# Performance work log

Measured on AMD Instinct MI355X. Metric: run time of the kernel, lower is better.

Reference implementation:

```python
import jax, jax.numpy as jnp
import numpy as np
import math

D = 128    # d_model
H = 8      # n_heads
NK = 16    # n_know
BS = 4
S = 256
DK = D // H
NEG = -1e32
LN_EPS = 1e-5


def _linear(x, W, b):
    return x @ W.T + b


def _layernorm(x, g, b):
    m = x.mean(-1, keepdims=True)
    v = ((x - m) ** 2).mean(-1, keepdims=True)
    return (x - m) / jnp.sqrt(v + LN_EPS) * g + b


def _attention(q, k, v, mask, gamma, maxout):
    # q,k,v: (B, H, S, DK); mask: (1,1,S,S) bool; gamma: (H,1,1)
    d_k = q.shape[-1]
    scores = jnp.einsum('bhid,bhjd->bhij', q, k) / math.sqrt(d_k)
    seqlen = scores.shape[-1]
    x = jnp.arange(seqlen, dtype=jnp.float32)
    pos = jnp.abs(x[None, :] - x[:, None])  # |j - i|, (S, S)
    # --- time-decay block (computed under no_grad in torch) ---
    s_ = jax.nn.softmax(jnp.where(mask, scores, NEG), axis=-1)
    distcum = jnp.cumsum(s_, axis=-1)
    disttotal = jnp.sum(s_, axis=-1, keepdims=True)
    dist = jnp.sqrt(jnp.clip((disttotal - distcum) * pos[None, None], 0.0, None))
    dist = jax.lax.stop_gradient(dist)
    effect = jnp.clip(jnp.exp(dist * (-jnp.abs(gamma)[None])), 1e-5, 1e5)
    scores = scores * effect
    scores = jax.nn.softmax(jnp.where(mask, scores, NEG), axis=-1)
    scores = jnp.where(mask, scores, 0.0)
    if maxout:
        scale = jnp.minimum(1.0 / scores.max(axis=-1, keepdims=True), 5.0)
        scores = scores * scale
    out = jnp.einsum('bhij,bhjd->bhid', scores, v)
    return out, scores


def _mha(q, k, v, mask, Wq, bq, Wk, bk, Wv, bv, Wo, bo, gamma, maxout):
    bs, seqlen, d = q.shape
    split = lambda x: x.reshape(bs, seqlen, H, DK).transpose(0, 2, 1, 3)
    qh = split(_linear(q, Wq, bq))
    kh = split(_linear(k, Wk, bk))
    vh = split(_linear(v, Wv, bv))
    out, scores = _attention(qh, kh, vh, mask, gamma, maxout)
    concat = out.transpose(0, 2, 1, 3).reshape(bs, seqlen, d)
    return _linear(concat, Wo, bo), scores


def _layer(query, key, values, peek_cur, Wq, bq, Wk, bk, Wv, bv, Wo, bo, gamma, lng, lnb):
    seqlen = query.shape[1]
    mask = jnp.tril(jnp.ones((seqlen, seqlen), bool), 0 if peek_cur else -1)[None, None]
    out, scores = _mha(query, key, values, mask, Wq, bq, Wk, bk, Wv, bv, Wo, bo, gamma,
                       maxout=not peek_cur)
    return _layernorm(query + out, lng, lnb), scores


def setup_inputs() -> dict:
    key = jax.random.key(0)
    ks = jax.random.split(key, 24)
    rn = lambda k, shape: (jax.random.normal(k, shape, jnp.float32) / math.sqrt(D))
    inp = {
        'q_emb': jax.random.normal(ks[0], (BS, S, D), jnp.float32),
        's_emb': jax.random.normal(ks[1], (BS, S, D), jnp.float32),
        'lens': jax.random.randint(ks[2], (BS,), 5, S),
        # block1 (kq_same=True -> shares Wq for K)
        'b1_Wq': rn(ks[3], (D, D)), 'b1_bq': jnp.zeros((D,), jnp.float32),
        'b1_Wv': rn(ks[4], (D, D)), 'b1_bv': jnp.zeros((D,), jnp.float32),
        'b1_Wo': rn(ks[5], (D, D)), 'b1_bo': jnp.zeros((D,), jnp.float32),
        'b1_gamma': jax.random.uniform(ks[6], (H, 1, 1), jnp.float32, -1.0, 1.0),
        'b1_lng': jnp.ones((D,), jnp.float32), 'b1_lnb': jnp.zeros((D,), jnp.float32),
        # block4 (kq_same=False)
        'b4_Wq': rn(ks[7], (D, D)), 'b4_bq': jnp.zeros((D,), jnp.float32),
        'b4_Wk': rn(ks[8], (D, D)), 'b4_bk': jnp.zeros((D,), jnp.float32),
        'b4_Wv': rn(ks[9], (D, D)), 'b4_bv': jnp.zeros((D,), jnp.float32),
        'b4_Wo': rn(ks[10], (D, D)), 'b4_bo': jnp.zeros((D,), jnp.float32),
        'b4_gamma': jax.random.uniform(ks[11], (H, 1, 1), jnp.float32, -1.0, 1.0),
        'b4_lng': jnp.ones((D,), jnp.float32), 'b4_lnb': jnp.zeros((D,), jnp.float32),
        'know_params': jax.random.uniform(ks[12], (NK, D), jnp.float32, -1.0, 1.0),
    }
    return inp


def reference(q_emb, s_emb, lens,
              b1_Wq, b1_bq, b1_Wv, b1_bv, b1_Wo, b1_bo, b1_gamma, b1_lng, b1_lnb,
              b4_Wq, b4_bq, b4_Wk, b4_bk, b4_Wv, b4_bv, b4_Wo, b4_bo, b4_gamma, b4_lng, b4_lnb,
              know_params):
    # n_layers == 1 path, eval mode (no mask dropout); lens unused in eval math.
    hq = q_emb
    p, q_scores = _layer(q_emb, q_emb, s_emb, True,
                         b1_Wq, b1_bq, b1_Wq, b1_bq, b1_Wv, b1_bv, b1_Wo, b1_bo,
                         b1_gamma, b1_lng, b1_lnb)
    bs, seqlen, d = p.shape
    query = jnp.broadcast_to(know_params[None, :, None, :], (bs, NK, seqlen, d)).reshape(bs * NK, seqlen, d)
    hq_r = jnp.broadcast_to(hq[:, None], (bs, NK, seqlen, d)).reshape(bs * NK, seqlen, d)
    p_r = jnp.broadcast_to(p[:, None], (bs, NK, seqlen, d)).reshape(bs * NK, seqlen, d)
    z, k_scores = _layer(query, hq_r, p_r, False,
                         b4_Wq, b4_bq, b4_Wk, b4_bk, b4_Wv, b4_bv, b4_Wo, b4_bo,
                         b4_gamma, b4_lng, b4_lnb)
    z = z.reshape(bs, NK, seqlen, d).transpose(0, 2, 1, 3).reshape(bs, seqlen, NK * d)
    k_scores = k_scores.reshape(bs, NK, H, seqlen, seqlen).transpose(0, 2, 3, 1, 4)
    return z, q_scores, k_scores
```

## Files before the change

### kernel.cpp

```cpp
#include <hip/hip_runtime.h>

#define DEV __device__ __forceinline__

DEV float4 f4fma(float4 a, float s, float4 w){
  a.x = fmaf(s, w.x, a.x); a.y = fmaf(s, w.y, a.y);
  a.z = fmaf(s, w.z, a.z); a.w = fmaf(s, w.w, a.w);
  return a;
}
DEV float4 f4add(float4 a, float4 b){
  a.x+=b.x; a.y+=b.y; a.z+=b.z; a.w+=b.w; return a;
}

DEV float waveAllMax(float x){
  #pragma unroll
  for(int o=1;o<64;o<<=1) x = fmaxf(x, __shfl_xor(x,o,64));
  return x;
}
DEV float waveAllSum(float x){
  #pragma unroll
  for(int o=1;o<64;o<<=1) x += __shfl_xor(x,o,64);
  return x;
}
DEV float waveReduceMax(float x){
  #pragma unroll
  for(int o=32;o>0;o>>=1) x = fmaxf(x, __shfl_down(x,o,64));
  return x;
}
DEV float blockMax256(float x, float* sc){
  int lane = threadIdx.x & 63, wid = threadIdx.x >> 6;
  x = waveReduceMax(x);
  __syncthreads();
  if(lane==0) sc[wid] = x;
  __syncthreads();
  return fmaxf(fmaxf(sc[0],sc[1]), fmaxf(sc[2],sc[3]));
}
DEV float blockScan256(float x, float* sc, float& total){
  int lane = threadIdx.x & 63, wid = threadIdx.x >> 6;
  float v = x;
  #pragma unroll
  for(int o=1;o<64;o<<=1){ float t = __shfl_up(v,o,64); if(lane>=o) v += t; }
  __syncthreads();
  if(lane==63) sc[wid] = v;
  __syncthreads();
  float pre=0.f, tot=0.f;
  #pragma unroll
  for(int ww=0;ww<4;ww++){ float s = sc[ww]; tot += s; if(ww<wid) pre += s; }
  total = tot;
  return v + pre;
}

template<int EPI>
DEV void gemm16_body(const float* __restrict__ in, const float* __restrict__ W,
                     const float* __restrict__ bias, const float* __restrict__ aux,
                     const float* __restrict__ lng, const float* __restrict__ lnb,
                     float* __restrict__ out, int r0, int nrows,
                     float* sWT, float (*sIn)[128])
{
  const int t = threadIdx.x;
  for(int idx=t; idx<2048; idx+=256){
    int r = idx>>7, c = idx&127;
    int row = r0+r;
    sIn[r][c] = (row<nrows) ? in[(size_t)row*128+c] : 0.f;
  }
  const int og = t & 31, rg = t >> 5;
  const int o0 = og*4;
  const float* s0p = sIn[rg*2];
  const float* s1p = sIn[rg*2+1];
  float4 a0 = make_float4(0,0,0,0), a1 = make_float4(0,0,0,0);

  #pragma unroll
  for(int half=0; half<2; half++){
    int c0 = half*64;
    __syncthreads();
    for(int idx=t; idx<8192; idx+=256){
      int o = idx>>6, cc = idx&63;
      sWT[cc*132 + o] = W[o*128 + c0 + cc];
    }
    __syncthreads();
    #pragma unroll 4
    for(int c=0;c<64;c+=4){
      float4 sA = *(const float4*)(s0p + c0 + c);
      float4 sB = *(const float4*)(s1p + c0 + c);
      const float* wp = sWT + c*132 + o0;
      float4 w0 = *(const float4*)(wp);
      float4 w1 = *(const float4*)(wp + 132);
      float4 w2 = *(const float4*)(wp + 264);
      float4 w3 = *(const float4*)(wp + 396);
      a0 = f4fma(a0, sA.x, w0); a0 = f4fma(a0, sA.y, w1);
      a0 = f4fma(a0, sA.z, w2); a0 = f4fma(a0, sA.w, w3);
      a1 = f4fma(a1, sB.x, w0); a1 = f4fma(a1, sB.y, w1);
      a1 = f4fma(a1, sB.z, w2); a1 = f4fma(a1, sB.w, w3);
    }
  }
  float4 bv = *(const float4*)(bias + o0);
  a0 = f4add(a0, bv); a1 = f4add(a1, bv);
  int row0 = r0 + rg*2, row1 = row0 + 1;

  if(EPI == 0){
    if(row0 < nrows) *(float4*)(out + (size_t)row0*128 + o0) = a0;
    if(row1 < nrows) *(float4*)(out + (size_t)row1*128 + o0) = a1;
  } else {
    const float* x0 = aux + ((row0>>8)&15)*128;
    const float* x1 = aux + ((row1>>8)&15)*128;
    a0 = f4add(a0, *(const float4*)(x0 + o0));
    a1 = f4add(a1, *(const float4*)(x1 + o0));
    float s0 = a0.x+a0.y+a0.z+a0.w, s1 = a1.x+a1.y+a1.z+a1.w;
    float q0 = a0.x*a0.x+a0.y*a0.y+a0.z*a0.z+a0.w*a0.w;
    float q1 = a1.x*a1.x+a1.y*a1.y+a1.z*a1.z+a1.w*a1.w;
    #pragma unroll
    for(int o=1;o<32;o<<=1){
      s0 += __shfl_xor(s0,o,64); q0 += __shfl_xor(q0,o,64);
      s1 += __shfl_xor(s1,o,64); q1 += __shfl_xor(q1,o,64);
    }
    float m0 = s0*0.0078125f, v0 = q0*0.0078125f - m0*m0;
    float m1 = s1*0.0078125f, v1 = q1*0.0078125f - m1*m1;
    float i0 = rsqrtf(v0+1e-5f), i1 = rsqrtf(v1+1e-5f);
    float4 g  = *(const float4*)(lng + o0);
    float4 b2 = *(const float4*)(lnb + o0);
    float4 y0, y1;
    y0.x=(a0.x-m0)*i0*g.x+b2.x; y0.y=(a0.y-m0)*i0*g.y+b2.y;
    y0.z=(a0.z-m0)*i0*g.z+b2.z; y0.w=(a0.w-m0)*i0*g.w+b2.w;
    y1.x=(a1.x-m1)*i1*g.x+b2.x; y1.y=(a1.y-m1)*i1*g.y+b2.y;
    y1.z=(a1.z-m1)*i1*g.z+b2.z; y1.w=(a1.w-m1)*i1*g.w+b2.w;
    int n0=(row0>>8)&15, b0=row0>>12, i0i=row0&255;
    int n1=(row1>>8)&15, b1=row1>>12, i1i=row1&255;
    float* p0 = out + ((((size_t)b0*256+i0i)*16+n0)<<7);
    float* p1 = out + ((((size_t)b1*256+i1i)*16+n1)<<7);
    *(float4*)(p0 + o0) = y0;
    *(float4*)(p1 + o0) = y1;
  }
}

template<int EPI>
__global__ __launch_bounds__(256) void gemm16_kernel(
  const float* __restrict__ in, const float* __restrict__ W,
  const float* __restrict__ bias, const float* __restrict__ aux,
  const float* __restrict__ lng, const float* __restrict__ lnb,
  float* __restrict__ out, int nrows)
{
  __shared__ float sWT[64*132];
  __shared__ float sIn[16][128];
  gemm16_body<EPI>(in, W, bias, aux, lng, lnb, out, blockIdx.x*16, nrows, sWT, sIn);
}

__global__ __launch_bounds__(256) void proj4_kernel(
  const float* __restrict__ in0, const float* __restrict__ W0, const float* __restrict__ b0, float* __restrict__ o0,
  const float* __restrict__ in1, const float* __restrict__ W1, const float* __restrict__ b1, float* __restrict__ o1,
  const float* __restrict__ in2, const float* __restrict__ W2, const float* __restrict__ b2, float* __restrict__ o2,
  const float* __restrict__ in3, const float* __restrict__ W3, const float* __restrict__ b3, float* __restrict__ o3)
{
  __shared__ float sWT[64*132];
  __shared__ float sIn[16][128];
  int bb = blockIdx.x;
  if(bb < 64)       gemm16_body<0>(in0,W0,b0,nullptr,nullptr,nullptr,o0, bb*16,      1024, sWT,sIn);
  else if(bb < 128) gemm16_body<0>(in1,W1,b1,nullptr,nullptr,nullptr,o1,(bb-64)*16,  1024, sWT,sIn);
  else if(bb < 192) gemm16_body<0>(in2,W2,b2,nullptr,nullptr,nullptr,o2,(bb-128)*16, 1024, sWT,sIn);
  else              gemm16_body<0>(in3,W3,b3,nullptr,nullptr,nullptr,o3, 0,          16,   sWT,sIn);
}

__global__ __launch_bounds__(256) void gemm_p_v4(
  const float* __restrict__ in, const float* __restrict__ Wo, const float* __restrict__ bo,
  const float* __restrict__ resid, const float* __restrict__ lng, const float* __restrict__ lnb,
  float* __restrict__ pout,
  const float* __restrict__ Wv, const float* __restrict__ bvv, float* __restrict__ v4out)
{
  __shared__ float sWT[64*132];
  __shared__ float sIn[16][128];
  const int t = threadIdx.x;
  const int r0 = blockIdx.x*16;
  for(int idx=t; idx<2048; idx+=256){
    int r = idx>>7, c = idx&127;
    sIn[r][c] = in[(size_t)(r0+r)*128+c];
  }
  const int og = t & 31, rg = t >> 5;
  const int o0 = og*4;
  const float* s0p = sIn[rg*2];
  const float* s1p = sIn[rg*2+1];
  float4 a0 = make_float4(0,0,0,0), a1 = make_float4(0,0,0,0);

  #pragma unroll
  for(int half=0; half<2; half++){
    int c0 = half*64;
    __syncthreads();
    for(int idx=t; idx<8192; idx+=256){
      int o = idx>>6, cc = idx&63;
      sWT[cc*132 + o] = Wo[o*128 + c0 + cc];
    }
    __syncthreads();
    #pragma unroll 4
    for(int c=0;c<64;c+=4){
      float4 sA = *(const float4*)(s0p + c0 + c);
      float4 sB = *(const float4*)(s1p + c0 + c);
      const float* wp = sWT + c*132 + o0;
      float4 w0 = *(const float4*)(wp);
      float4 w1 = *(const float4*)(wp + 132);
      float4 w2 = *(const float4*)(wp + 264);
      float4 w3 = *(const float4*)(wp + 396);
      a0 = f4fma(a0, sA.x, w0); a0 = f4fma(a0, sA.y, w1);
      a0 = f4fma(a0, sA.z, w2); a0 = f4fma(a0, sA.w, w3);
      a1 = f4fma(a1, sB.x, w0); a1 = f4fma(a1, sB.y, w1);
      a1 = f4fma(a1, sB.z, w2); a1 = f4fma(a1, sB.w, w3);
    }
  }
  int row0 = r0 + rg*2, row1 = row0 + 1;
  {
    float4 bv = *(const float4*)(bo + o0);
    a0 = f4add(a0, bv); a1 = f4add(a1, bv);
    a0 = f4add(a0, *(const float4*)(resid + (size_t)row0*128 + o0));
    a1 = f4add(a1, *(const float4*)(resid + (size_t)row1*128 + o0));
    float s0 = a0.x+a0.y+a0.z+a0.w, s1 = a1.x+a1.y+a1.z+a1.w;
    float q0 = a0.x*a0.x+a0.y*a0.y+a0.z*a0.z+a0.w*a0.w;
    float q1 = a1.x*a1.x+a1.y*a1.y+a1.z*a1.z+a1.w*a1.w;
    #pragma unroll
    for(int o=1;o<32;o<<=1){
      s0 += __shfl_xor(s0,o,64); q0 += __shfl_xor(q0,o,64);
      s1 += __shfl_xor(s1,o,64); q1 += __shfl_xor(q1,o,64);
    }
    float m0 = s0*0.0078125f, v0 = q0*0.0078125f - m0*m0;
    float m1 = s1*0.0078125f, v1 = q1*0.0078125f - m1*m1;
    float i0 = rsqrtf(v0+1e-5f), i1 = rsqrtf(v1+1e-5f);
    float4 g  = *(const float4*)(lng + o0);
    float4 b2 = *(const float4*)(lnb + o0);
    float4 y0, y1;
    y0.x=(a0.x-m0)*i0*g.x+b2.x; y0.y=(a0.y-m0)*i0*g.y+b2.y;
    y0.z=(a0.z-m0)*i0*g.z+b2.z; y0.w=(a0.w-m0)*i0*g.w+b2.w;
    y1.x=(a1.x-m1)*i1*g.x+b2.x; y1.y=(a1.y-m1)*i1*g.y+b2.y;
    y1.z=(a1.z-m1)*i1*g.z+b2.z; y1.w=(a1.w-m1)*i1*g.w+b2.w;
    *(float4*)(pout + (size_t)row0*128 + o0) = y0;
    *(float4*)(pout + (size_t)row1*128 + o0) = y1;
    __syncthreads();
    *(float4*)&sIn[rg*2  ][o0] = y0;
    *(float4*)&sIn[rg*2+1][o0] = y1;
  }

  a0 = make_float4(0,0,0,0); a1 = make_float4(0,0,0,0);
  #pragma unroll
  for(int half=0; half<2; half++){
    int c0 = half*64;
    __syncthreads();
    for(int idx=t; idx<8192; idx+=256){
      int o = idx>>6, cc = idx&63;
      sWT[cc*132 + o] = Wv[o*128 + c0 + cc];
    }
    __syncthreads();
    #pragma unroll 4
    for(int c=0;c<64;c+=4){
      float4 sA = *(const float4*)(s0p + c0 + c);
      float4 sB = *(const float4*)(s1p + c0 + c);
      const float* wp = sWT + c*132 + o0;
      float4 w0 = *(const float4*)(wp);
      float4 w1 = *(const float4*)(wp + 132);
      float4 w2 = *(const float4*)(wp + 264);
      float4 w3 = *(const float4*)(wp + 396);
      a0 = f4fma(a0, sA.x, w0); a0 = f4fma(a0, sA.y, w1);
      a0 = f4fma(a0, sA.z, w2); a0 = f4fma(a0, sA.w, w3);
      a1 = f4fma(a1, sB.x, w0); a1 = f4fma(a1, sB.y, w1);
      a1 = f4fma(a1, sB.z, w2); a1 = f4fma(a1, sB.w, w3);
    }
  }
  float4 bv2 = *(const float4*)(bvv + o0);
  a0 = f4add(a0, bv2); a1 = f4add(a1, bv2);
  *(float4*)(v4out + (size_t)row0*128 + o0) = a0;
  *(float4*)(v4out + (size_t)row1*128 + o0) = a1;
}

__global__ __launch_bounds__(256) void attn1_kernel(
  const float* __restrict__ qk, const float* __restrict__ v1,
  const float* __restrict__ gamma, float* __restrict__ qs, float* __restrict__ aout)
{
  __shared__ float psW[4][256];
  int tile = blockIdx.x & 15;
  int bh   = blockIdx.x >> 4;
  int b = bh >> 3, h = bh & 7;
  int t = threadIdx.x, lane = t & 63, w = t >> 6;
  int d = lane & 15, jg = lane >> 4;
  int j0 = 4*lane;

  float4 kreg[4][4];
  #pragma unroll
  for(int u=0;u<4;u++){
    const float4* kr = (const float4*)(qk + (b*256 + j0 + u)*128 + h*16);
    kreg[u][0]=kr[0]; kreg[u][1]=kr[1]; kreg[u][2]=kr[2]; kreg[u][3]=kr[3];
  }
  float vreg[64];
  const float* vbase = v1 + (b*256 + jg*64)*128 + h*16 + d;
  #pragma unroll
  for(int k=0;k<64;k++) vreg[k] = vbase[k*128];

  float ga = fabsf(gamma[h]);

  for(int r=0;r<4;r++){
    int i = tile*16 + w*4 + r;
    const float4* qr = (const float4*)(qk + (b*256 + i)*128 + h*16);
    float4 q0=qr[0], q1=qr[1], q2=qr[2], q3=qr[3];

    float raw[4]; float mloc = -3e38f;
    #pragma unroll
    for(int u=0;u<4;u++){
      const float4* kk = kreg[u];
      float s = q0.x*kk[0].x + q0.y*kk[0].y + q0.z*kk[0].z + q0.w*kk[0].w
              + q1.x*kk[1].x + q1.y*kk[1].y + q1.z*kk[1].z + q1.w*kk[1].w
              + q2.x*kk[2].x + q2.y*kk[2].y + q2.z*kk[2].z + q2.w*kk[2].w
              + q3.x*kk[3].x + q3.y*kk[3].y + q3.z*kk[3].z + q3.w*kk[3].w;
      raw[u] = s * 0.25f;
      if(j0+u <= i) mloc = fmaxf(mloc, raw[u]);
    }
    float m1 = waveAllMax(mloc);
    float e[4], c[4]; float lsum = 0.f;
    #pragma unroll
    for(int u=0;u<4;u++){
      e[u] = (j0+u <= i) ? __expf(raw[u]-m1) : 0.f;
      lsum += e[u]; c[u] = lsum;
    }
    float s = lsum;
    #pragma unroll
    for(int o=1;o<64;o<<=1){ float tv = __shfl_up(s,o,64); if(lane>=o) s += tv; }
    float pre = s - lsum;
    float tot = __shfl(s, 63, 64);
    float invtot = 1.f/tot;

    float s2v[4]; float m2loc = -3e38f;
    #pragma unroll
    for(int u=0;u<4;u++){
      int j = j0+u;
      float cum  = (pre + c[u]) * invtot;
      float remn = fmaxf(1.f - cum, 0.f);
      float dist = sqrtf(remn * fabsf((float)(j - i)));
      float eff  = fminf(fmaxf(__expf(-ga*dist), 1e-5f), 1e5f);
      s2v[u] = raw[u]*eff;
      if(j <= i) m2loc = fmaxf(m2loc, s2v[u]);
    }
    float m2 = waveAllMax(m2loc);
    float e2[4]; float zloc = 0.f;
    #pragma unroll
    for(int u=0;u<4;u++){
      e2[u] = (j0+u <= i) ? __expf(s2v[u]-m2) : 0.f;
      zloc += e2[u];
    }
    float Z = waveAllSum(zloc);
    float invZ = 1.f/Z;
    float p0=e2[0]*invZ, p1=e2[1]*invZ, p2=e2[2]*invZ, p3=e2[3]*invZ;

    *(float4*)(qs + ((size_t)(bh*256 + i))*256 + j0) = make_float4(p0,p1,p2,p3);

    *(float4*)&psW[w][j0] = make_float4(p0,p1,p2,p3);
    float acc = 0.f;
    const float4* pw = (const float4*)&psW[w][jg*64];
    #pragma unroll
    for(int k=0;k<16;k++){
      float4 pk = pw[k];
      acc += pk.x*vreg[4*k] + pk.y*vreg[4*k+1] + pk.z*vreg[4*k+2] + pk.w*vreg[4*k+3];
    }
    acc += __shfl_xor(acc,16,64);
    acc += __shfl_xor(acc,32,64);
    if(lane < 16)
      aout[(b*256 + i)*128 + h*16 + d] = acc;
  }
}

DEV float dot16(const float* a, const float* b){
  float s = 0.f;
  #pragma unroll
  for(int k=0;k<16;k++) s += a[k]*b[k];
  return s;
}

__global__ __launch_bounds__(256) void attn4_main(
  const float* __restrict__ q4, const float* __restrict__ k4,
  const float* __restrict__ v4, const float* __restrict__ gamma,
  float* __restrict__ ks, float* __restrict__ aout)
{
  __shared__ float sc4[4];
  __shared__ float rawL[256];
  __shared__ float PL[256];
  __shared__ float psW[4][256];
  int half = blockIdx.x & 1;
  int bnh  = blockIdx.x >> 1;
  int b = bnh >> 7, n = (bnh >> 3) & 15, h = bnh & 7;
  int t = threadIdx.x, lane = t & 63, w = t >> 6;
  int d = lane & 15, jg = lane >> 4;
  int j0 = 4*lane;

  {
    const float* qrow = q4 + n*128 + h*16;
    const float* krow = k4 + (b*256 + t)*128 + h*16;
    float raw = dot16(qrow, krow) * 0.25f;
    float M = blockMax256(raw, sc4);
    float E = __expf(raw - M);
    float tot;
    float P = blockScan256(E, sc4, tot);
    rawL[t] = raw;
    PL[t]   = P;
  }
  float vreg[64];
  const float* vbase = v4 + (b*256 + jg*64)*128 + h*16 + d;
  #pragma unroll
  for(int k=0;k<64;k++) vreg[k] = vbase[k*128];
  __syncthreads();

  float4 rw = *(const float4*)(rawL + j0);
  float4 Pv = *(const float4*)(PL + j0);
  float P_[4] = {Pv.x, Pv.y, Pv.z, Pv.w};
  float R_[4] = {rw.x, rw.y, rw.z, rw.w};

  float g4a = fabsf(gamma[h]);
  size_t ksrowbase = ((size_t)(b*8 + h)*256)*4096 + (size_t)n*256 + j0;

  for(int r=0;r<32;r++){
    int i = half*128 + w*32 + r;
    float p0=0.f,p1=0.f,p2=0.f,p3=0.f;
    if(i > 0){
      float invPm1 = 1.f / PL[i-1];
      float s2v[4]; float mloc = -3e38f;
      #pragma unroll
      for(int u=0;u<4;u++){
        int j = j0+u;
        float cum  = P_[u]*invPm1;
        float remn = fmaxf(1.f - cum, 0.f);
        float dist = sqrtf(remn * fabsf((float)(j - i)));
        float eff  = fminf(fmaxf(__expf(-g4a*dist), 1e-5f), 1e5f);
        float s2   = R_[u]*eff;
        s2v[u] = s2;
        if(j < i) mloc = fmaxf(mloc, s2);
      }
      float m2 = waveAllMax(mloc);
      float e_[4]; float zloc = 0.f;
      #pragma unroll
      for(int u=0;u<4;u++){
        float e = (j0+u < i) ? __expf(s2v[u]-m2) : 0.f;
        e_[u] = e; zloc += e;
      }
      float Z = waveAllSum(zloc);
      float sc = fminf(5.f/Z, 1.f);
      p0=e_[0]*sc; p1=e_[1]*sc; p2=e_[2]*sc; p3=e_[3]*sc;
    }
    *(float4*)(ks + ksrowbase + (size_t)i*4096) = make_float4(p0,p1,p2,p3);

    *(float4*)&psW[w][j0] = make_float4(p0,p1,p2,p3);
    float acc = 0.f;
    const float4* pw = (const float4*)&psW[w][jg*64];
    #pragma unroll
    for(int k=0;k<16;k++){
      float4 pk = pw[k];
      acc += pk.x*vreg[4*k] + pk.y*vreg[4*k+1] + pk.z*vreg[4*k+2] + pk.w*vreg[4*k+3];
    }
    acc += __shfl_xor(acc,16,64);
    acc += __shfl_xor(acc,32,64);
    if(lane < 16)
      aout[((b*16+n)*256 + i)*128 + h*16 + d] = acc;
  }
}

extern "C" void kernel_launch(void* const* d_in, const int* in_sizes, int n_in,
                              void* d_out, int out_size, void* d_ws, size_t ws_size,
                              hipStream_t stream)
{
  (void)in_sizes; (void)n_in; (void)out_size; (void)ws_size;
  const float* q_emb   = (const float*)d_in[0];
  const float* s_emb   = (const float*)d_in[1];
  const float* b1_Wq   = (const float*)d_in[3];
  const float* b1_bq   = (const float*)d_in[4];
  const float* b1_Wv   = (const float*)d_in[5];
  const float* b1_bv   = (const float*)d_in[6];
  const float* b1_Wo   = (const float*)d_in[7];
  const float* b1_bo   = (const float*)d_in[8];
  const float* b1_gamma= (const float*)d_in[9];
  const float* b1_lng  = (const float*)d_in[10];
  const float* b1_lnb  = (const float*)d_in[11];
  const float* b4_Wq   = (const float*)d_in[12];
  const float* b4_bq   = (const float*)d_in[13];
  const float* b4_Wk   = (const float*)d_in[14];
  const float* b4_bk   = (const float*)d_in[15];
  const float* b4_Wv   = (const float*)d_in[16];
  const float* b4_bv   = (const float*)d_in[17];
  const float* b4_Wo   = (const float*)d_in[18];
  const float* b4_bo   = (const float*)d_in[19];
  const float* b4_gamma= (const float*)d_in[20];
  const float* b4_lng  = (const float*)d_in[21];
  const float* b4_lnb  = (const float*)d_in[22];
  const float* know    = (const float*)d_in[23];

  float* w    = (float*)d_ws;
  float* qk1  = w;
  float* v1   = w + 131072;
  float* a1o  = w + 262144;
  float* p    = w + 393216;
  float* q4   = w + 524288;
  float* k4   = w + 526336;
  float* v4   = w + 657408;
  float* a4o  = w + 788480;

  float* z_out  = (float*)d_out;
  float* qs_out = z_out + 2097152;
  float* ks_out = z_out + 4194304;

  proj4_kernel<<<193,256,0,stream>>>(
      q_emb, b1_Wq, b1_bq, qk1,
      s_emb, b1_Wv, b1_bv, v1,
      q_emb, b4_Wk, b4_bk, k4,
      know,  b4_Wq, b4_bq, q4);

  attn1_kernel<<<512,256,0,stream>>>(qk1, v1, b1_gamma, qs_out, a1o);

  gemm_p_v4<<<64,256,0,stream>>>(a1o, b1_Wo, b1_bo, q_emb, b1_lng, b1_lnb, p,
                                 b4_Wv, b4_bv, v4);

  attn4_main<<<1024,256,0,stream>>>(q4, k4, v4, b4_gamma, ks_out, a4o);

  gemm16_kernel<2><<<1024,256,0,stream>>>(a4o, b4_Wo, b4_bo, know, b4_lng, b4_lnb, z_out, 16384);
}
```

Measured before the change: 305.0 us.

## Vectorize P·V with float4 V registers and split attn4 rows into quarters

In both attention kernels the P·V product now has each lane hold 16 consecutive key rows times 4 head dims as float4, instead of 64 strided scalars. Probabilities go to padded shared memory (stride 20) to avoid bank conflicts, and a float4 shuffle reduction across 16 lane groups produces the output, written as one float4. This replaces 64 strided scalar loads with 16 vector loads. attn4 also splits each (b,n,h) across 4 blocks instead of 2, doubling the grid to 2048. That adds parallelism but repeats the per-block prefix scan and V load more often, and the reduction needs more shuffles.

```diff
diff --git a/kernel.cpp b/kernel.cpp
--- a/kernel.cpp
+++ b/kernel.cpp
@@ -268,12 +268,12 @@
   const float* __restrict__ qk, const float* __restrict__ v1,
   const float* __restrict__ gamma, float* __restrict__ qs, float* __restrict__ aout)
 {
-  __shared__ float psW[4][256];
+  __shared__ float psW[4][320];
   int tile = blockIdx.x & 15;
   int bh   = blockIdx.x >> 4;
   int b = bh >> 3, h = bh & 7;
   int t = threadIdx.x, lane = t & 63, w = t >> 6;
-  int d = lane & 15, jg = lane >> 4;
+  int d4 = lane & 3, jg = lane >> 2;
   int j0 = 4*lane;
 
   float4 kreg[4][4];
@@ -282,12 +282,14 @@
     const float4* kr = (const float4*)(qk + (b*256 + j0 + u)*128 + h*16);
     kreg[u][0]=kr[0]; kreg[u][1]=kr[1]; kreg[u][2]=kr[2]; kreg[u][3]=kr[3];
   }
-  float vreg[64];
-  const float* vbase = v1 + (b*256 + jg*64)*128 + h*16 + d;
-  #pragma unroll
-  for(int k=0;k<64;k++) vreg[k] = vbase[k*128];
+  float4 vreg[16];
+  #pragma unroll
+  for(int jj=0;jj<16;jj++)
+    vreg[jj] = *(const float4*)(v1 + (b*256 + jg*16 + jj)*128 + h*16 + d4*4);
 
   float ga = fabsf(gamma[h]);
+  float* myChunk = &psW[w][(lane>>2)*20 + 4*(lane&3)];
+  const float* pw = &psW[w][jg*20];
 
   for(int r=0;r<4;r++){
     int i = tile*16 + w*4 + r;
@@ -343,18 +345,23 @@
 
     *(float4*)(qs + ((size_t)(bh*256 + i))*256 + j0) = make_float4(p0,p1,p2,p3);
 
-    *(float4*)&psW[w][j0] = make_float4(p0,p1,p2,p3);
-    float acc = 0.f;
-    const float4* pw = (const float4*)&psW[w][jg*64];
-    #pragma unroll
-    for(int k=0;k<16;k++){
-      float4 pk = pw[k];
-      acc += pk.x*vreg[4*k] + pk.y*vreg[4*k+1] + pk.z*vreg[4*k+2] + pk.w*vreg[4*k+3];
-    }
-    acc += __shfl_xor(acc,16,64);
-    acc += __shfl_xor(acc,32,64);
-    if(lane < 16)
-      aout[(b*256 + i)*128 + h*16 + d] = acc;
+    *(float4*)myChunk = make_float4(p0,p1,p2,p3);
+    float4 acc = make_float4(0,0,0,0);
+    #pragma unroll
+    for(int k=0;k<4;k++){
+      float4 pk = *(const float4*)(pw + 4*k);
+      acc = f4fma(acc, pk.x, vreg[4*k  ]);
+      acc = f4fma(acc, pk.y, vreg[4*k+1]);
+      acc = f4fma(acc, pk.z, vreg[4*k+2]);
+      acc = f4fma(acc, pk.w, vreg[4*k+3]);
+    }
+    #pragma unroll
+    for(int o=4;o<64;o<<=1){
+      acc.x += __shfl_xor(acc.x,o,64); acc.y += __shfl_xor(acc.y,o,64);
+      acc.z += __shfl_xor(acc.z,o,64); acc.w += __shfl_xor(acc.w,o,64);
+    }
+    if(lane < 4)
+      *(float4*)(aout + (b*256 + i)*128 + h*16 + lane*4) = acc;
   }
 }
 
@@ -373,12 +380,12 @@
   __shared__ float sc4[4];
   __shared__ float rawL[256];
   __shared__ float PL[256];
-  __shared__ float psW[4][256];
-  int half = blockIdx.x & 1;
-  int bnh  = blockIdx.x >> 1;
+  __shared__ float psW[4][320];
+  int quarter = blockIdx.x & 3;
+  int bnh  = blockIdx.x >> 2;
   int b = bnh >> 7, n = (bnh >> 3) & 15, h = bnh & 7;
   int t = threadIdx.x, lane = t & 63, w = t >> 6;
-  int d = lane & 15, jg = lane >> 4;
+  int d4 = lane & 3, jg = lane >> 2;
   int j0 = 4*lane;
 
   {
@@ -392,10 +399,10 @@
     rawL[t] = raw;
     PL[t]   = P;
   }
-  float vreg[64];
-  const float* vbase = v4 + (b*256 + jg*64)*128 + h*16 + d;
-  #pragma unroll
-  for(int k=0;k<64;k++) vreg[k] = vbase[k*128];
+  float4 vreg[16];
+  #pragma unroll
+  for(int jj=0;jj<16;jj++)
+    vreg[jj] = *(const float4*)(v4 + (b*256 + jg*16 + jj)*128 + h*16 + d4*4);
   __syncthreads();
 
   float4 rw = *(const float4*)(rawL + j0);
@@ -405,9 +412,11 @@
 
   float g4a = fabsf(gamma[h]);
   size_t ksrowbase = ((size_t)(b*8 + h)*256)*4096 + (size_t)n*256 + j0;
-
-  for(int r=0;r<32;r++){
-    int i = half*128 + w*32 + r;
+  float* myChunk = &psW[w][(lane>>2)*20 + 4*(lane&3)];
+  const float* pw = &psW[w][jg*20];
+
+  for(int r=0;r<16;r++){
+    int i = quarter*64 + w*16 + r;
     float p0=0.f,p1=0.f,p2=0.f,p3=0.f;
     if(i > 0){
       float invPm1 = 1.f / PL[i-1];
@@ -436,18 +445,23 @@
     }
     *(float4*)(ks + ksrowbase + (size_t)i*4096) = make_float4(p0,p1,p2,p3);
 
-    *(float4*)&psW[w][j0] = make_float4(p0,p1,p2,p3);
-    float acc = 0.f;
-    const float4* pw = (const float4*)&psW[w][jg*64];
-    #pragma unroll
-    for(int k=0;k<16;k++){
-      float4 pk = pw[k];
-      acc += pk.x*vreg[4*k] + pk.y*vreg[4*k+1] + pk.z*vreg[4*k+2] + pk.w*vreg[4*k+3];
-    }
-    acc += __shfl_xor(acc,16,64);
-    acc += __shfl_xor(acc,32,64);
-    if(lane < 16)
-      aout[((b*16+n)*256 + i)*128 + h*16 + d] = acc;
+    *(float4*)myChunk = make_float4(p0,p1,p2,p3);
+    float4 acc = make_float4(0,0,0,0);
+    #pragma unroll
+    for(int k=0;k<4;k++){
+      float4 pk = *(const float4*)(pw + 4*k);
+      acc = f4fma(acc, pk.x, vreg[4*k  ]);
+      acc = f4fma(acc, pk.y, vreg[4*k+1]);
+      acc = f4fma(acc, pk.z, vreg[4*k+2]);
+      acc = f4fma(acc, pk.w, vreg[4*k+3]);
+    }
+    #pragma unroll
+    for(int o=4;o<64;o<<=1){
+      acc.x += __shfl_xor(acc.x,o,64); acc.y += __shfl_xor(acc.y,o,64);
+      acc.z += __shfl_xor(acc.z,o,64); acc.w += __shfl_xor(acc.w,o,64);
+    }
+    if(lane < 4)
+      *(float4*)(aout + ((b*16+n)*256 + i)*128 + h*16 + lane*4) = acc;
   }
 }
 
@@ -505,7 +519,7 @@
   gemm_p_v4<<<64,256,0,stream>>>(a1o, b1_Wo, b1_bo, q_emb, b1_lng, b1_lnb, p,
                                  b4_Wv, b4_bv, v4);
 
-  attn4_main<<<1024,256,0,stream>>>(q4, k4, v4, b4_gamma, ks_out, a4o);
+  attn4_main<<<2048,256,0,stream>>>(q4, k4, v4, b4_gamma, ks_out, a4o);
 
   gemm16_kernel<2><<<1024,256,0,stream>>>(a4o, b4_Wo, b4_bo, know, b4_lng, b4_lnb, z_out, 16384);
 }
```

Result: no change. 304.1 us (-0.3%).
